# Kernel tuning notes

Hardware: AMD Instinct MI355X
Metric: run time of the kernel (lower is better)

## Reference

```python
import jax, jax.numpy as jnp
import numpy as np

HID = 1024
INTER = 4096
RDIM = 128          # expert_retrieval_size
HEADS = 4
NUM_EXPERTS = 16384
NUM_KEYS = 128      # sqrt(NUM_EXPERTS)
TOPK = 8            # num_cdmoe_experts_per_head
B, T = 2, 2048


def setup_inputs() -> dict:
    key = jax.random.key(0)
    ks = jax.random.split(key, 8)
    s = lambda fan_in: 1.0 / np.sqrt(fan_in)
    return {
        "hidden_states": jax.random.normal(ks[0], (B, T, HID), jnp.float32),
        "Wq": jax.random.normal(ks[1], (HEADS * RDIM, HID), jnp.float32) * s(HID),
        "keys": jax.random.normal(ks[2], (HEADS, NUM_KEYS, 2, RDIM // 2), jnp.float32) * s(RDIM // 2),
        "down_embed": jax.random.normal(ks[3], (NUM_EXPERTS, HID), jnp.float32) * 0.02,
        "up_embed": jax.random.normal(ks[4], (NUM_EXPERTS, HID), jnp.float32) * 0.02,
        "Wg": jax.random.normal(ks[5], (INTER, HID), jnp.float32) * s(HID),
        "Wu": jax.random.normal(ks[6], (INTER, HID), jnp.float32) * s(HID),
        "Wd": jax.random.normal(ks[7], (HID, INTER), jnp.float32) * s(INTER),
    }


def reference(hidden_states, Wq, keys, down_embed, up_embed, Wg, Wu, Wd):
    b, t, _ = hidden_states.shape
    # product-key retrieval
    q = hidden_states @ Wq.T                                   # [b,t,h*rdim]
    q = q.reshape(b, t, 2, HEADS, RDIM // 2)                   # [b,t,2,h,n]
    q = jnp.transpose(q, (2, 0, 1, 3, 4))                      # [2,b,t,h,n]
    sim = jnp.einsum('pbthn,hkpn->pbthk', q, keys)             # [2,b,t,h,K]
    sx, ix = jax.lax.top_k(sim[0], TOPK)                       # [b,t,h,k]
    sy, iy = jax.lax.top_k(sim[1], TOPK)
    all_scores = (sx[..., :, None] + sy[..., None, :]).reshape(b, t, HEADS, TOPK * TOPK)
    all_indices = (ix[..., :, None] * NUM_KEYS + iy[..., None, :]).reshape(b, t, HEADS, TOPK * TOPK)
    scores, pk = jax.lax.top_k(all_scores, TOPK)               # [b,t,h,k]
    indices = jnp.take_along_axis(all_indices, pk, axis=-1)    # [b,t,h,k]
    # gather expert embeddings and combine
    down = down_embed[indices]                                 # [b,t,h,k,d]
    up = up_embed[indices]                                     # [b,t,h,k,d]
    w = jnp.einsum('btd,bthkd->bthk', hidden_states, down)
    w = jax.nn.silu(w) * jax.nn.softmax(scores, axis=-1)
    experts_states = jnp.einsum('bthk,bthkd->btd', w, up)
    # dense MLP
    mlp = (jax.nn.silu(hidden_states @ Wg.T) * (hidden_states @ Wu.T)) @ Wd.T
    return mlp + experts_states
```

## Files before the change

### kernel.cpp

```cpp
#include <hip/hip_runtime.h>

#define NTOK 4096
#define HID 1024
#define QDIM 512
#define HEADS 4
#define NKEYS 128
#define TOPK 8
#define INTERDIM 4096

typedef __bf16 bf16x8 __attribute__((ext_vector_type(8)));
typedef __bf16 bf16x4 __attribute__((ext_vector_type(4)));
typedef float f32x4 __attribute__((ext_vector_type(4)));

__device__ __forceinline__ float siluf(float x) { return x / (1.f + __expf(-x)); }
__device__ __forceinline__ unsigned sortable(float f) {
  unsigned u = __float_as_uint(f);
  return (u & 0x80000000u) ? ~u : (u | 0x80000000u);
}
__device__ __forceinline__ float bfl(unsigned u) { return __uint_as_float(u << 16); }
__device__ __forceinline__ float bfh(unsigned u) { return __uint_as_float(u & 0xFFFF0000u); }

#define GLD_LDS16(g, l)                                                                   \
  __builtin_amdgcn_global_load_lds(                                                      \
      (const __attribute__((address_space(1))) unsigned int*)(g),                        \
      (__attribute__((address_space(3))) unsigned int*)(l), 16, 0, 0)

__device__ __forceinline__ void cast_one_f4(const float* __restrict__ src,
                                            __bf16* __restrict__ dst, int i)
{
  const float4 v = ((const float4*)src)[i];
  bf16x4 o;
  o[0] = (__bf16)v.x; o[1] = (__bf16)v.y; o[2] = (__bf16)v.z; o[3] = (__bf16)v.w;
  ((bf16x4*)dst)[i] = o;
}

__global__ __launch_bounds__(256) void cast5_kernel(
    const float* __restrict__ hs, const float* __restrict__ wq,
    const float* __restrict__ wg, const float* __restrict__ wu,
    const float* __restrict__ wd,
    __bf16* __restrict__ hs_o, __bf16* __restrict__ wq_o,
    __bf16* __restrict__ wg_o, __bf16* __restrict__ wu_o,
    __bf16* __restrict__ wd_o)
{
  int b = blockIdx.x;
  const float* src; __bf16* dst;
  if      (b < 4096)  { src = hs; dst = hs_o; }
  else if (b < 4608)  { src = wq; dst = wq_o; b -= 4096; }
  else if (b < 8704)  { src = wg; dst = wg_o; b -= 4608; }
  else if (b < 12800) { src = wu; dst = wu_o; b -= 8704; }
  else                { src = wd; dst = wd_o; b -= 12800; }
  cast_one_f4(src, dst, b * 256 + threadIdx.x);
}

__global__ __launch_bounds__(256) void cast2_kernel(
    const float* __restrict__ dwe, const float* __restrict__ upe,
    __bf16* __restrict__ dwe_o, __bf16* __restrict__ upe_o)
{
  int b = blockIdx.x;
  const float* src; __bf16* dst;
  if (b < 16384) { src = dwe; dst = dwe_o; }
  else           { src = upe; dst = upe_o; b -= 16384; }
  cast_one_f4(src, dst, b * 256 + threadIdx.x);
}

__global__ __launch_bounds__(256) void cast_keys_kernel(const float* __restrict__ keys,
                                                        __bf16* __restrict__ kbf)
{
  const int i = blockIdx.x * 256 + threadIdx.x;
  const int n = i & 63, p = (i >> 6) & 1, k = (i >> 7) & 127, h = (i >> 14) & 3;
  kbf[(((size_t)(p * 4 + h) * NKEYS) + k) * 64 + n] = (__bf16)keys[i];
}

template<bool DUAL, bool OUT_BF16>
__global__ __launch_bounds__(512) void gemm_mfma(
    const __bf16* __restrict__ A, const __bf16* __restrict__ B0,
    const __bf16* __restrict__ B1, void* __restrict__ Cv,
    int M, int N, int K, int BW, int BH, int NRX)
{
  __shared__ __attribute__((aligned(16))) __bf16 As [128 * 32];
  __shared__ __attribute__((aligned(16))) __bf16 Bs0[128 * 32];
  __shared__ __attribute__((aligned(16))) __bf16 Bs1[DUAL ? 128 * 32 : 8];

  const int bid = blockIdx.y * gridDim.x + blockIdx.x;
  const int xcd = bid & 7, idx = bid >> 3;
  const int rx = (xcd % NRX) * BW;
  const int ry = (xcd / NRX) * BH;
  const int bx = rx + idx % BW;
  const int by = ry + idx / BW;

  const int tid  = threadIdx.x;
  const int wave = tid >> 6;
  const int lane = tid & 63;
  const int m0 = by * 128;
  const int n0 = bx * 128;
  const int wr = wave >> 2, wc = wave & 3;
  const int lhi = lane >> 4, llo = lane & 15;

  f32x4 acc0[4][2] = {};
  f32x4 acc1[4][2] = {};

  const int r0 = tid >> 2, col0 = (tid & 3) * 8;
  __bf16* ldsA  = &As [(size_t)wave * 512];
  __bf16* ldsB0 = &Bs0[(size_t)wave * 512];
  __bf16* ldsB1 = &Bs1[(size_t)wave * 512];

  for (int k0 = 0; k0 < K; k0 += 32) {
    GLD_LDS16(A  + (size_t)(m0 + r0) * K + k0 + col0, ldsA);
    GLD_LDS16(B0 + (size_t)(n0 + r0) * K + k0 + col0, ldsB0);
    if constexpr (DUAL)
      GLD_LDS16(B1 + (size_t)(n0 + r0) * K + k0 + col0, ldsB1);
    __syncthreads();

    bf16x8 afr[4], bfr0[2], bfr1[2];
#pragma unroll
    for (int mi = 0; mi < 4; ++mi)
      afr[mi] = *(const bf16x8*)&As[(wr * 64 + mi * 16 + llo) * 32 + lhi * 8];
#pragma unroll
    for (int nj = 0; nj < 2; ++nj)
      bfr0[nj] = *(const bf16x8*)&Bs0[(wc * 32 + nj * 16 + llo) * 32 + lhi * 8];
    if constexpr (DUAL) {
#pragma unroll
      for (int nj = 0; nj < 2; ++nj)
        bfr1[nj] = *(const bf16x8*)&Bs1[(wc * 32 + nj * 16 + llo) * 32 + lhi * 8];
    }
#pragma unroll
    for (int mi = 0; mi < 4; ++mi)
#pragma unroll
      for (int nj = 0; nj < 2; ++nj) {
        acc0[mi][nj] = __builtin_amdgcn_mfma_f32_16x16x32_bf16(afr[mi], bfr0[nj], acc0[mi][nj], 0, 0, 0);
        if constexpr (DUAL)
          acc1[mi][nj] = __builtin_amdgcn_mfma_f32_16x16x32_bf16(afr[mi], bfr1[nj], acc1[mi][nj], 0, 0, 0);
      }
    __syncthreads();
  }

#pragma unroll
  for (int mi = 0; mi < 4; ++mi)
#pragma unroll
    for (int nj = 0; nj < 2; ++nj)
#pragma unroll
      for (int r = 0; r < 4; ++r) {
        const int row = m0 + wr * 64 + mi * 16 + lhi * 4 + r;
        const int col = n0 + wc * 32 + nj * 16 + llo;
        float v = acc0[mi][nj][r];
        if constexpr (DUAL) v = siluf(v) * acc1[mi][nj][r];
        if constexpr (OUT_BF16) ((__bf16*)Cv)[(size_t)row * N + col] = (__bf16)v;
        else                    ((float*) Cv)[(size_t)row * N + col] = v;
      }
}

__global__ __launch_bounds__(256) void sims_gemm(
    const __bf16* __restrict__ Qbf,
    const __bf16* __restrict__ Kbf,
    float* __restrict__ S)
{
  __shared__ __attribute__((aligned(16))) __bf16 As[128 * 32];
  __shared__ __attribute__((aligned(16))) __bf16 Bs[128 * 32];

  const int z = blockIdx.y;
  const int p = z >> 2, h = z & 3;
  const __bf16* A = Qbf + p * 256 + h * 64;
  const __bf16* B = Kbf + (size_t)z * NKEYS * 64;
  float* C = S + (size_t)z * NTOK * NKEYS;

  const int tid  = threadIdx.x;
  const int wave = tid >> 6;
  const int lane = tid & 63;
  const int m0 = blockIdx.x * 128;
  const int wr = wave >> 1, wc = wave & 1;
  const int lhi = lane >> 4, llo = lane & 15;

  f32x4 acc[4][4] = {};

  const int c0 = tid, c1 = 256 + tid;
  const int r0 = c0 >> 2, col0 = (c0 & 3) * 8;
  const int r1 = c1 >> 2, col1 = (c1 & 3) * 8;
  __bf16* ldsA0 = &As[(wave * 64) * 8];
  __bf16* ldsA1 = &As[(256 + wave * 64) * 8];
  __bf16* ldsB0 = &Bs[(wave * 64) * 8];
  __bf16* ldsB1 = &Bs[(256 + wave * 64) * 8];

  for (int k0 = 0; k0 < 64; k0 += 32) {
    GLD_LDS16(A + (size_t)(m0 + r0) * 512 + k0 + col0, ldsA0);
    GLD_LDS16(A + (size_t)(m0 + r1) * 512 + k0 + col1, ldsA1);
    GLD_LDS16(B + (size_t)r0 * 64 + k0 + col0, ldsB0);
    GLD_LDS16(B + (size_t)r1 * 64 + k0 + col1, ldsB1);
    __syncthreads();

    bf16x8 afr[4], bfr[4];
#pragma unroll
    for (int mi = 0; mi < 4; ++mi)
      afr[mi] = *(const bf16x8*)&As[(wr * 64 + mi * 16 + llo) * 32 + lhi * 8];
#pragma unroll
    for (int nj = 0; nj < 4; ++nj)
      bfr[nj] = *(const bf16x8*)&Bs[(wc * 64 + nj * 16 + llo) * 32 + lhi * 8];
#pragma unroll
    for (int mi = 0; mi < 4; ++mi)
#pragma unroll
      for (int nj = 0; nj < 4; ++nj)
        acc[mi][nj] = __builtin_amdgcn_mfma_f32_16x16x32_bf16(afr[mi], bfr[nj], acc[mi][nj], 0, 0, 0);
    __syncthreads();
  }

#pragma unroll
  for (int mi = 0; mi < 4; ++mi)
#pragma unroll
    for (int nj = 0; nj < 4; ++nj)
#pragma unroll
      for (int r = 0; r < 4; ++r) {
        const int row = m0 + wr * 64 + mi * 16 + lhi * 4 + r;
        const int col = wc * 64 + nj * 16 + llo;
        C[(size_t)row * NKEYS + col] = acc[mi][nj][r];
      }
}

__global__ __launch_bounds__(256) void topk_kernel(
    const float* __restrict__ S,
    int* __restrict__ out_idx,
    float* __restrict__ out_prob)
{
  const int g = blockIdx.x;
  const int h = blockIdx.y;
  const int t = threadIdx.x;
  const int tok0 = g * 16;

  __shared__ float    sims  [16][2][128];
  __shared__ unsigned packed[16][2][128];
  __shared__ unsigned cmax  [16][2][8];
  __shared__ int      cnt   [16][2];
  __shared__ unsigned char surv[16][2][128];
  __shared__ float    stv   [16][2][8];
  __shared__ unsigned char sti[16][2][8];
  __shared__ unsigned cnd   [16][64];

  const int ltok = t >> 4, j0 = (t & 15) * 8;
  unsigned pk[2][8];
#pragma unroll
  for (int p = 0; p < 2; ++p) {
    const float* src = S + (((size_t)(p * 4 + h) * NTOK) + tok0 + ltok) * NKEYS + j0;
    const float4 a = ((const float4*)src)[0];
    const float4 b = ((const float4*)src)[1];
    float v[8] = {a.x, a.y, a.z, a.w, b.x, b.y, b.z, b.w};
#pragma unroll
    for (int e = 0; e < 8; ++e) {
      const unsigned u = (sortable(v[e]) & 0xFFFFFF80u) | (unsigned)(127 - (j0 + e));
      sims  [ltok][p][j0 + e] = v[e];
      packed[ltok][p][j0 + e] = u;
      pk[p][e] = u;
    }
  }
  if (t < 32) cnt[t >> 1][t & 1] = 0;
  __syncthreads();

  {
    const int ctok = t >> 4, cp = (t >> 3) & 1, c = t & 7;
    const uint4* q = (const uint4*)&packed[ctok][cp][c * 16];
    unsigned m = 0;
#pragma unroll
    for (int r = 0; r < 4; ++r) {
      const uint4 u = q[r];
      m = max(m, max(max(u.x, u.y), max(u.z, u.w)));
    }
    cmax[ctok][cp][c] = m;
  }
  __syncthreads();

#pragma unroll
  for (int p = 0; p < 2; ++p) {
    const uint4* cm = (const uint4*)&cmax[ltok][p][0];
    const uint4 ca = cm[0], cb = cm[1];
    const unsigned t0 = min(min(min(ca.x, ca.y), min(ca.z, ca.w)),
                            min(min(cb.x, cb.y), min(cb.z, cb.w)));
#pragma unroll
    for (int e = 0; e < 8; ++e) {
      if (pk[p][e] >= t0) {
        const int s = atomicAdd(&cnt[ltok][p], 1);
        surv[ltok][p][s] = (unsigned char)(j0 + e);
      }
    }
  }
  __syncthreads();

  {
    const int gid = t >> 3, lane8 = t & 7;
    const int stok = gid >> 1, sp = gid & 1;
    const int n = cnt[stok][sp];
    const uint4* row = (const uint4*)&packed[stok][sp][0];
    for (int s = lane8; s < n; s += 8) {
      const int j = surv[stok][sp][s];
      const unsigned mypk = packed[stok][sp][j];
      int rk = 0;
#pragma unroll 8
      for (int q4 = 0; q4 < 32; ++q4) {
        const uint4 u = row[q4];
        rk += (u.x > mypk) + (u.y > mypk) + (u.z > mypk) + (u.w > mypk);
      }
      if (rk < TOPK) {
        stv[stok][sp][rk] = sims[stok][sp][j];
        sti[stok][sp][rk] = (unsigned char)j;
      }
    }
  }
  __syncthreads();

  const int w = t >> 6, l = t & 63;
  for (int round = 0; round < 4; ++round) {
    const int tok = w * 4 + round;
    const int ci = l >> 3, cj = l & 7;
    const float cv = stv[tok][0][ci] + stv[tok][1][cj];
    const unsigned cpk = (sortable(cv) & 0xFFFFFFC0u) | (unsigned)(63 - l);
    cnd[tok][l] = cpk;
    __syncthreads();
    int rk = 0;
    const uint4* row = (const uint4*)&cnd[tok][0];
#pragma unroll
    for (int q4 = 0; q4 < 16; ++q4) {
      const uint4 u = row[q4];
      rk += (u.x > cpk) + (u.y > cpk) + (u.z > cpk) + (u.w > cpk);
    }
    float mx = cv;
#pragma unroll
    for (int off = 32; off; off >>= 1) mx = fmaxf(mx, __shfl_xor(mx, off));
    const float e = (rk < TOPK) ? __expf(cv - mx) : 0.f;
    float sum = e;
#pragma unroll
    for (int off = 32; off; off >>= 1) sum += __shfl_xor(sum, off);
    if (rk < TOPK) {
      const int o = ((tok0 + tok) * HEADS + h) * TOPK + rk;
      out_idx [o] = (int)sti[tok][0][ci] * NKEYS + (int)sti[tok][1][cj];
      out_prob[o] = e / sum;
    }
  }
}

__global__ __launch_bounds__(256) void expert_kernel(
    const float* __restrict__ hs,
    const __bf16* __restrict__ down_e,
    const __bf16* __restrict__ up_e,
    const int* __restrict__ idx,
    const float* __restrict__ prob,
    float* __restrict__ out)
{
  const int token = blockIdx.x;
  const int t = threadIdx.x, w = t >> 6, l = t & 63;
  __shared__ float4 sred[4][256];

  const float4* hrow = (const float4*)(hs + (size_t)token * HID);
  const float4 h0 = hrow[2 * l], h1 = hrow[2 * l + 1];
  const float4 h2 = hrow[128 + 2 * l], h3 = hrow[128 + 2 * l + 1];
  float4 a0 = {0,0,0,0}, a1 = {0,0,0,0}, a2 = {0,0,0,0}, a3 = {0,0,0,0};

  const int*   tidx  = idx  + token * 32 + w * 8;
  const float* tprob = prob + token * 32 + w * 8;
#pragma unroll 2
  for (int e = 0; e < 8; ++e) {
    const int   ex = tidx[e];
    const float p  = tprob[e];
    const uint4* dr = (const uint4*)(down_e + (size_t)ex * HID);
    const uint4 dA = dr[l], dB = dr[64 + l];
    float part = h0.x * bfl(dA.x) + h0.y * bfh(dA.x) + h0.z * bfl(dA.y) + h0.w * bfh(dA.y)
               + h1.x * bfl(dA.z) + h1.y * bfh(dA.z) + h1.z * bfl(dA.w) + h1.w * bfh(dA.w)
               + h2.x * bfl(dB.x) + h2.y * bfh(dB.x) + h2.z * bfl(dB.y) + h2.w * bfh(dB.y)
               + h3.x * bfl(dB.z) + h3.y * bfh(dB.z) + h3.z * bfl(dB.w) + h3.w * bfh(dB.w);
#pragma unroll
    for (int off = 32; off; off >>= 1) part += __shfl_xor(part, off);
    const float wgt = siluf(part) * p;
    const uint4* ur = (const uint4*)(up_e + (size_t)ex * HID);
    const uint4 uA = ur[l], uB = ur[64 + l];
    a0.x += wgt * bfl(uA.x); a0.y += wgt * bfh(uA.x); a0.z += wgt * bfl(uA.y); a0.w += wgt * bfh(uA.y);
    a1.x += wgt * bfl(uA.z); a1.y += wgt * bfh(uA.z); a1.z += wgt * bfl(uA.w); a1.w += wgt * bfh(uA.w);
    a2.x += wgt * bfl(uB.x); a2.y += wgt * bfh(uB.x); a2.z += wgt * bfl(uB.y); a2.w += wgt * bfh(uB.y);
    a3.x += wgt * bfl(uB.z); a3.y += wgt * bfh(uB.z); a3.z += wgt * bfl(uB.w); a3.w += wgt * bfh(uB.w);
  }
  sred[w][2 * l] = a0; sred[w][2 * l + 1] = a1;
  sred[w][128 + 2 * l] = a2; sred[w][128 + 2 * l + 1] = a3;
  __syncthreads();

  const float4 r0 = sred[0][t], r1 = sred[1][t], r2 = sred[2][t], r3 = sred[3][t];
  float4* o = (float4*)(out + (size_t)token * HID);
  float4 cur = o[t];
  cur.x += r0.x + r1.x + r2.x + r3.x;
  cur.y += r0.y + r1.y + r2.y + r3.y;
  cur.z += r0.z + r1.z + r2.z + r3.z;
  cur.w += r0.w + r1.w + r2.w + r3.w;
  o[t] = cur;
}

extern "C" void kernel_launch(void* const* d_in, const int* in_sizes, int n_in,
                              void* d_out, int out_size, void* d_ws, size_t ws_size,
                              hipStream_t stream)
{
  const float* hs   = (const float*)d_in[0];
  const float* Wq   = (const float*)d_in[1];
  const float* keys = (const float*)d_in[2];
  const float* dwe  = (const float*)d_in[3];
  const float* upe  = (const float*)d_in[4];
  const float* Wg   = (const float*)d_in[5];
  const float* Wu   = (const float*)d_in[6];
  const float* Wd   = (const float*)d_in[7];
  float* out = (float*)d_out;

  __bf16* qbf     = (__bf16*)d_ws;
  __bf16* kbf     = qbf + (size_t)NTOK * QDIM;
  int*    idxb    = (int*)(kbf + 8 * NKEYS * 64);
  float*  probb   = (float*)(idxb + NTOK * HEADS * TOPK);
  __bf16* hs_bf   = (__bf16*)(probb + NTOK * HEADS * TOPK);
  __bf16* wq_bf   = hs_bf + (size_t)NTOK * HID;
  __bf16* wg_bf   = wq_bf + (size_t)QDIM * HID;
  __bf16* wu_bf   = wg_bf + (size_t)INTERDIM * HID;
  __bf16* wd_bf   = wu_bf + (size_t)INTERDIM * HID;
  __bf16* interbf = wd_bf + (size_t)HID * INTERDIM;
  float*  simsb   = (float*)interbf;
  __bf16* dwe_bf  = interbf;
  __bf16* upe_bf  = hs_bf;

  cast5_kernel<<<16896, 256, 0, stream>>>(hs, Wq, Wg, Wu, Wd,
                                          hs_bf, wq_bf, wg_bf, wu_bf, wd_bf);
  cast_keys_kernel<<<256, 256, 0, stream>>>(keys, kbf);

  gemm_mfma<false, true><<<dim3(QDIM / 128, NTOK / 128), 512, 0, stream>>>(
      hs_bf, wq_bf, nullptr, qbf, NTOK, QDIM, HID, 4, 4, 1);

  sims_gemm<<<dim3(NTOK / 128, 8), 256, 0, stream>>>(qbf, kbf, simsb);
  topk_kernel<<<dim3(NTOK / 16, HEADS), 256, 0, stream>>>(simsb, idxb, probb);

  gemm_mfma<true, true><<<dim3(INTERDIM / 128, NTOK / 128), 512, 0, stream>>>(
      hs_bf, wg_bf, wu_bf, interbf, NTOK, INTERDIM, HID, 8, 16, 4);

  gemm_mfma<false, false><<<dim3(HID / 128, NTOK / 128), 512, 0, stream>>>(
      interbf, wd_bf, nullptr, out, NTOK, HID, INTERDIM, 8, 4, 1);

  cast2_kernel<<<32768, 256, 0, stream>>>(dwe, upe, dwe_bf, upe_bf);
  expert_kernel<<<NTOK, 256, 0, stream>>>(hs, dwe_bf, upe_bf, idxb, probb, out);
}
```

Before: 344.1 us.

## Triple-buffer LDS tiles in MFMA GEMM to overlap global loads with compute

Replaces the single-buffered load/sync/compute loop in the bf16 MFMA GEMM with a three-stage LDS ring. Tiles are prefetched two iterations ahead via global_load_lds, and explicit vmcnt waits plus one barrier per iteration replace the two __syncthreads. This is meant to hide global memory latency behind MFMA work in the dense MLP GEMMs. The cost is triple the LDS footprint, which may reduce occupancy, and reliance on manual waitcnt accounting being correct.

```diff
diff --git a/kernel.cpp b/kernel.cpp
--- a/kernel.cpp
+++ b/kernel.cpp
@@ -77,9 +77,9 @@
     const __bf16* __restrict__ B1, void* __restrict__ Cv,
     int M, int N, int K, int BW, int BH, int NRX)
 {
-  __shared__ __attribute__((aligned(16))) __bf16 As [128 * 32];
-  __shared__ __attribute__((aligned(16))) __bf16 Bs0[128 * 32];
-  __shared__ __attribute__((aligned(16))) __bf16 Bs1[DUAL ? 128 * 32 : 8];
+  __shared__ __attribute__((aligned(16))) __bf16 As [3][128 * 32];
+  __shared__ __attribute__((aligned(16))) __bf16 Bs0[3][128 * 32];
+  __shared__ __attribute__((aligned(16))) __bf16 Bs1[DUAL ? 3 : 1][DUAL ? 128 * 32 : 8];
 
   const int bid = blockIdx.y * gridDim.x + blockIdx.x;
   const int xcd = bid & 7, idx = bid >> 3;
@@ -100,28 +100,43 @@
   f32x4 acc1[4][2] = {};
 
   const int r0 = tid >> 2, col0 = (tid & 3) * 8;
-  __bf16* ldsA  = &As [(size_t)wave * 512];
-  __bf16* ldsB0 = &Bs0[(size_t)wave * 512];
-  __bf16* ldsB1 = &Bs1[(size_t)wave * 512];
-
-  for (int k0 = 0; k0 < K; k0 += 32) {
-    GLD_LDS16(A  + (size_t)(m0 + r0) * K + k0 + col0, ldsA);
-    GLD_LDS16(B0 + (size_t)(n0 + r0) * K + k0 + col0, ldsB0);
-    if constexpr (DUAL)
-      GLD_LDS16(B1 + (size_t)(n0 + r0) * K + k0 + col0, ldsB1);
-    __syncthreads();
+  const __bf16* Ag  = A  + (size_t)(m0 + r0) * K + col0;
+  const __bf16* B0g = B0 + (size_t)(n0 + r0) * K + col0;
+  const __bf16* B1g = DUAL ? (B1 + (size_t)(n0 + r0) * K + col0) : nullptr;
+  const size_t ldsoff = (size_t)wave * 512;
+
+  const int NT = K >> 5;
+  constexpr int LPT = DUAL ? 3 : 2;
+
+#define STAGE_TILE(t)                                                  \
+  do {                                                                 \
+    const int _b = (t) % 3;                                            \
+    const int _k = (t) * 32;                                           \
+    GLD_LDS16(Ag  + _k, &As [_b][ldsoff]);                             \
+    GLD_LDS16(B0g + _k, &Bs0[_b][ldsoff]);                             \
+    if constexpr (DUAL) GLD_LDS16(B1g + _k, &Bs1[_b][ldsoff]);         \
+  } while (0)
+
+  STAGE_TILE(0);
+  STAGE_TILE(1);
+  asm volatile("s_waitcnt vmcnt(%0)" :: "i"(LPT) : "memory");
+  __builtin_amdgcn_s_barrier();
+
+  for (int t = 0; t < NT; ++t) {
+    if (t + 2 < NT) STAGE_TILE(t + 2);
+    const int b = t % 3;
 
     bf16x8 afr[4], bfr0[2], bfr1[2];
 #pragma unroll
     for (int mi = 0; mi < 4; ++mi)
-      afr[mi] = *(const bf16x8*)&As[(wr * 64 + mi * 16 + llo) * 32 + lhi * 8];
+      afr[mi] = *(const bf16x8*)&As[b][(wr * 64 + mi * 16 + llo) * 32 + lhi * 8];
 #pragma unroll
     for (int nj = 0; nj < 2; ++nj)
-      bfr0[nj] = *(const bf16x8*)&Bs0[(wc * 32 + nj * 16 + llo) * 32 + lhi * 8];
+      bfr0[nj] = *(const bf16x8*)&Bs0[b][(wc * 32 + nj * 16 + llo) * 32 + lhi * 8];
     if constexpr (DUAL) {
 #pragma unroll
       for (int nj = 0; nj < 2; ++nj)
-        bfr1[nj] = *(const bf16x8*)&Bs1[(wc * 32 + nj * 16 + llo) * 32 + lhi * 8];
+        bfr1[nj] = *(const bf16x8*)&Bs1[b][(wc * 32 + nj * 16 + llo) * 32 + lhi * 8];
     }
 #pragma unroll
     for (int mi = 0; mi < 4; ++mi)
@@ -131,8 +146,12 @@
         if constexpr (DUAL)
           acc1[mi][nj] = __builtin_amdgcn_mfma_f32_16x16x32_bf16(afr[mi], bfr1[nj], acc1[mi][nj], 0, 0, 0);
       }
-    __syncthreads();
-  }
+
+    if (t + 2 < NT)      asm volatile("s_waitcnt vmcnt(%0)" :: "i"(LPT) : "memory");
+    else if (t + 1 < NT) asm volatile("s_waitcnt vmcnt(0)" ::: "memory");
+    __builtin_amdgcn_s_barrier();
+  }
+#undef STAGE_TILE
 
 #pragma unroll
   for (int mi = 0; mi < 4; ++mi)
```

After: 351.8 us. 2.2% more time.

## Split-K the down-projection GEMM and fold the partial sum into the expert kernel

Applied to the files above, without the earlier changes.

The down-projection GEMM is split into two K halves using a third grid dimension, which doubles the block count so the GPU has more parallelism to fill its CUs. The first half writes fp32 to the output as before. The second half writes a bf16 partial to a new workspace buffer, and the expert kernel adds that partial while it accumulates into the output. This adds an extra write and read of a 4096x1024 bf16 buffer and rounds half the K reduction to bf16. The split path runs only when the workspace is large enough; otherwise the original launch is used.

```diff
diff --git a/kernel.cpp b/kernel.cpp
--- a/kernel.cpp
+++ b/kernel.cpp
@@ -74,8 +74,8 @@
 template<bool DUAL, bool OUT_BF16>
 __global__ __launch_bounds__(512) void gemm_mfma(
     const __bf16* __restrict__ A, const __bf16* __restrict__ B0,
-    const __bf16* __restrict__ B1, void* __restrict__ Cv,
-    int M, int N, int K, int BW, int BH, int NRX)
+    const __bf16* __restrict__ B1, void* __restrict__ Cv, __bf16* __restrict__ Cv1,
+    int M, int N, int K, int LD, int BW, int BH, int NRX)
 {
   __shared__ __attribute__((aligned(16))) __bf16 As [128 * 32];
   __shared__ __attribute__((aligned(16))) __bf16 Bs0[128 * 32];
@@ -87,6 +87,8 @@
   const int ry = (xcd / NRX) * BH;
   const int bx = rx + idx % BW;
   const int by = ry + idx / BW;
+
+  const int kz = blockIdx.z * K;
 
   const int tid  = threadIdx.x;
   const int wave = tid >> 6;
@@ -100,15 +102,18 @@
   f32x4 acc1[4][2] = {};
 
   const int r0 = tid >> 2, col0 = (tid & 3) * 8;
+  const __bf16* Ag  = A  + kz + (size_t)(m0 + r0) * LD + col0;
+  const __bf16* B0g = B0 + kz + (size_t)(n0 + r0) * LD + col0;
+  const __bf16* B1g = DUAL ? (B1 + kz + (size_t)(n0 + r0) * LD + col0) : nullptr;
   __bf16* ldsA  = &As [(size_t)wave * 512];
   __bf16* ldsB0 = &Bs0[(size_t)wave * 512];
   __bf16* ldsB1 = &Bs1[(size_t)wave * 512];
 
   for (int k0 = 0; k0 < K; k0 += 32) {
-    GLD_LDS16(A  + (size_t)(m0 + r0) * K + k0 + col0, ldsA);
-    GLD_LDS16(B0 + (size_t)(n0 + r0) * K + k0 + col0, ldsB0);
+    GLD_LDS16(Ag  + k0, ldsA);
+    GLD_LDS16(B0g + k0, ldsB0);
     if constexpr (DUAL)
-      GLD_LDS16(B1 + (size_t)(n0 + r0) * K + k0 + col0, ldsB1);
+      GLD_LDS16(B1g + k0, ldsB1);
     __syncthreads();
 
     bf16x8 afr[4], bfr0[2], bfr1[2];
@@ -144,8 +149,12 @@
         const int col = n0 + wc * 32 + nj * 16 + llo;
         float v = acc0[mi][nj][r];
         if constexpr (DUAL) v = siluf(v) * acc1[mi][nj][r];
-        if constexpr (OUT_BF16) ((__bf16*)Cv)[(size_t)row * N + col] = (__bf16)v;
-        else                    ((float*) Cv)[(size_t)row * N + col] = v;
+        if constexpr (OUT_BF16) {
+          ((__bf16*)Cv)[(size_t)row * N + col] = (__bf16)v;
+        } else {
+          if (blockIdx.z == 0) ((float*)Cv)[(size_t)row * N + col] = v;
+          else                 Cv1[(size_t)row * N + col] = (__bf16)v;
+        }
       }
 }
 
@@ -333,12 +342,14 @@
   }
 }
 
+template<bool SPLIT>
 __global__ __launch_bounds__(256) void expert_kernel(
     const float* __restrict__ hs,
     const __bf16* __restrict__ down_e,
     const __bf16* __restrict__ up_e,
     const int* __restrict__ idx,
     const float* __restrict__ prob,
+    const __bf16* __restrict__ p1,
     float* __restrict__ out)
 {
   const int token = blockIdx.x;
@@ -379,6 +390,11 @@
   const float4 r0 = sred[0][t], r1 = sred[1][t], r2 = sred[2][t], r3 = sred[3][t];
   float4* o = (float4*)(out + (size_t)token * HID);
   float4 cur = o[t];
+  if constexpr (SPLIT) {
+    const uint2 pb = ((const uint2*)(p1 + (size_t)token * HID))[t];
+    cur.x += bfl(pb.x); cur.y += bfh(pb.x);
+    cur.z += bfl(pb.y); cur.w += bfh(pb.y);
+  }
   cur.x += r0.x + r1.x + r2.x + r3.x;
   cur.y += r0.y + r1.y + r2.y + r3.y;
   cur.z += r0.z + r1.z + r2.z + r3.z;
@@ -410,26 +426,38 @@
   __bf16* wu_bf   = wg_bf + (size_t)INTERDIM * HID;
   __bf16* wd_bf   = wu_bf + (size_t)INTERDIM * HID;
   __bf16* interbf = wd_bf + (size_t)HID * INTERDIM;
+  __bf16* p1      = interbf + (size_t)NTOK * INTERDIM;
   float*  simsb   = (float*)interbf;
   __bf16* dwe_bf  = interbf;
   __bf16* upe_bf  = hs_bf;
 
+  const size_t need_split = ((size_t)((char*)(p1 + (size_t)NTOK * HID) - (char*)d_ws));
+  const bool split = ws_size >= need_split;
+
   cast5_kernel<<<16896, 256, 0, stream>>>(hs, Wq, Wg, Wu, Wd,
                                           hs_bf, wq_bf, wg_bf, wu_bf, wd_bf);
   cast_keys_kernel<<<256, 256, 0, stream>>>(keys, kbf);
 
   gemm_mfma<false, true><<<dim3(QDIM / 128, NTOK / 128), 512, 0, stream>>>(
-      hs_bf, wq_bf, nullptr, qbf, NTOK, QDIM, HID, 4, 4, 1);
+      hs_bf, wq_bf, nullptr, qbf, nullptr, NTOK, QDIM, HID, HID, 4, 4, 1);
 
   sims_gemm<<<dim3(NTOK / 128, 8), 256, 0, stream>>>(qbf, kbf, simsb);
   topk_kernel<<<dim3(NTOK / 16, HEADS), 256, 0, stream>>>(simsb, idxb, probb);
 
   gemm_mfma<true, true><<<dim3(INTERDIM / 128, NTOK / 128), 512, 0, stream>>>(
-      hs_bf, wg_bf, wu_bf, interbf, NTOK, INTERDIM, HID, 8, 16, 4);
-
-  gemm_mfma<false, false><<<dim3(HID / 128, NTOK / 128), 512, 0, stream>>>(
-      interbf, wd_bf, nullptr, out, NTOK, HID, INTERDIM, 8, 4, 1);
+      hs_bf, wg_bf, wu_bf, interbf, nullptr, NTOK, INTERDIM, HID, HID, 8, 16, 4);
+
+  if (split) {
+    gemm_mfma<false, false><<<dim3(HID / 128, NTOK / 128, 2), 512, 0, stream>>>(
+        interbf, wd_bf, nullptr, out, p1, NTOK, HID, INTERDIM / 2, INTERDIM, 8, 4, 1);
+  } else {
+    gemm_mfma<false, false><<<dim3(HID / 128, NTOK / 128), 512, 0, stream>>>(
+        interbf, wd_bf, nullptr, out, nullptr, NTOK, HID, INTERDIM, INTERDIM, 8, 4, 1);
+  }
 
   cast2_kernel<<<32768, 256, 0, stream>>>(dwe, upe, dwe_bf, upe_bf);
-  expert_kernel<<<NTOK, 256, 0, stream>>>(hs, dwe_bf, upe_bf, idxb, probb, out);
-}
+  if (split)
+    expert_kernel<true><<<NTOK, 256, 0, stream>>>(hs, dwe_bf, upe_bf, idxb, probb, p1, out);
+  else
+    expert_kernel<false><<<NTOK, 256, 0, stream>>>(hs, dwe_bf, upe_bf, idxb, probb, nullptr, out);
+}
```

Measured after the change: 326.1 us. 5.2% less time.
